# Kernel optimization log

Measured on AMD Instinct MI355X. Metric: run time of the kernel, lower is better.

## Reference

```python
import jax, jax.numpy as jnp
import numpy as np

B, N, DIM = 2, 2048, 1024
HEADS, DIM_HEAD = 16, 64
INNER = HEADS * DIM_HEAD  # 1024


def setup_inputs() -> dict:
    key = jax.random.key(0)
    k1, k2, k3, k4 = jax.random.split(key, 4)
    x = jax.random.normal(k1, (B, N, DIM), dtype=jnp.float32)
    # Linear weights (stored as [in, out] so y = x @ W)
    Wq = jax.random.normal(k2, (DIM, INNER), dtype=jnp.float32) * (DIM ** -0.5)
    Wkv = jax.random.normal(k3, (DIM, INNER * 2), dtype=jnp.float32) * (DIM ** -0.5)
    Wo = jax.random.normal(k4, (INNER, DIM), dtype=jnp.float32) * (INNER ** -0.5)
    return {"x": x, "Wq": Wq, "Wkv": Wkv, "Wo": Wo}


def reference(x, Wq, Wkv, Wo):
    # q/k/v projections (no bias), split heads: b n (h d) -> b h n d
    b, n, _ = x.shape
    q = (x @ Wq).reshape(b, n, HEADS, DIM_HEAD).transpose(0, 2, 1, 3)
    kv = x @ Wkv
    k, v = jnp.split(kv, 2, axis=-1)
    k = k.reshape(b, n, HEADS, DIM_HEAD).transpose(0, 2, 1, 3)
    v = v.reshape(b, n, HEADS, DIM_HEAD).transpose(0, 2, 1, 3)

    scale = DIM_HEAD ** -0.5
    scores = jnp.einsum('bhid,bhjd->bhij', q, k) * scale  # [b,h,n,n]
    # causal mask: positions j > i masked with most-negative value (as in torch impl)
    max_neg = -jnp.finfo(scores.dtype).max
    causal_mask = jnp.triu(jnp.ones((n, n), dtype=bool), k=1)
    scores = jnp.where(causal_mask, max_neg, scores)
    p = jax.nn.softmax(scores, axis=-1)
    out = jnp.einsum('bhij,bhjd->bhid', p, v)  # [b,h,n,d]
    out = out.transpose(0, 2, 1, 3).reshape(b, n, INNER)
    return out @ Wo
```

## Files before the change

kernel.cpp:

```cpp
#include <hip/hip_runtime.h>
#include <cstdint>


typedef __bf16 bf16_t;
typedef __bf16 bf16x8 __attribute__((ext_vector_type(8)));
typedef __bf16 bf16x4 __attribute__((ext_vector_type(4)));
typedef float  f32x4  __attribute__((ext_vector_type(4)));
typedef float  f32x16 __attribute__((ext_vector_type(16)));
typedef unsigned int u32;

#define QSCALE 0.18033688011112042f


__device__ __forceinline__ float fast_exp2(float x) {
#if __has_builtin(__builtin_amdgcn_exp2f)
  return __builtin_amdgcn_exp2f(x);
#else
  return exp2f(x);
#endif
}

__device__ __forceinline__ void swap32(u32& a, u32& b) {
#if __has_builtin(__builtin_amdgcn_permlane32_swap)
  typedef unsigned int u32x2 __attribute__((ext_vector_type(2)));
  const u32x2 r = __builtin_amdgcn_permlane32_swap(a, b, false, false);
  a = r[0]; b = r[1];
#else
  const u32 xa = (u32)__shfl_xor((int)a, 32, 64);
  const u32 xb = (u32)__shfl_xor((int)b, 32, 64);
  const bool hi = (threadIdx.x & 32) != 0;
  const u32 r0 = hi ? xb : a;
  const u32 r1 = hi ? b : xa;
  a = r0; b = r1;
#endif
}

__device__ __forceinline__ void gload_lds16(const void* gsrc, void* ldst) {
  __builtin_amdgcn_global_load_lds(
      (__attribute__((address_space(1))) void*)(uintptr_t)gsrc,
      (__attribute__((address_space(3))) void*)(uintptr_t)(uint32_t)(uintptr_t)ldst,
      16, 0, 0);
}

__device__ __forceinline__ u32 pkbf(float a, float b) {
  const u32 lo = (u32)__builtin_bit_cast(unsigned short, (bf16_t)a);
  const u32 hi = (u32)__builtin_bit_cast(unsigned short, (bf16_t)b);
  return (hi << 16) | lo;
}

__global__ __launch_bounds__(256) void cvt_kernel(const float* __restrict__ in,
                                                  bf16_t* __restrict__ out) {
  const int idx = (blockIdx.x * 256 + threadIdx.x) * 4;
  const float4 v = *(const float4*)(in + idx);
  bf16x4 o;
  o[0] = (bf16_t)v.x; o[1] = (bf16_t)v.y; o[2] = (bf16_t)v.z; o[3] = (bf16_t)v.w;
  *(bf16x4*)(out + idx) = o;
}

__global__ __launch_bounds__(256) void transpose_kernel(const float* __restrict__ W,
                                                        bf16_t* __restrict__ Wt,
                                                        int K, int Nn) {
  __shared__ float tile[32][33];
  const int bx = blockIdx.x, by = blockIdx.y;
  const int x = bx * 32 + threadIdx.x;
  #pragma unroll
  for (int r0 = 0; r0 < 32; r0 += 8) {
    const int r = r0 + threadIdx.y;
    tile[r][threadIdx.x] = W[(size_t)(by * 32 + r) * Nn + x];
  }
  __syncthreads();
  const int xo = by * 32 + threadIdx.x;
  #pragma unroll
  for (int r0 = 0; r0 < 32; r0 += 8) {
    const int r = r0 + threadIdx.y;
    Wt[(size_t)(bx * 32 + r) * K + xo] = (bf16_t)tile[threadIdx.x][r];
  }
}

template <int MODE>
__global__ __launch_bounds__(256) void gemm_kernel(
    const bf16_t* __restrict__ A, const bf16_t* __restrict__ Bt,
    bf16_t* __restrict__ outQ, bf16_t* __restrict__ outK,
    bf16_t* __restrict__ outV, float* __restrict__ outf) {
  constexpr int KD = 1024;
  __shared__ bf16_t As[2][128][64];
  __shared__ bf16_t Bs[2][128][64];
  const int t = threadIdx.x;
  const int lane = t & 63, w = t >> 6;
  const int wr = w >> 1, wc = w & 1;
  const int lrow = lane & 15, lq = lane >> 4;
  const int bm = blockIdx.y * 128, bn = blockIdx.x * 128;

  f32x4 acc[4][4] = {};

  auto stage = [&](int buf, int k0) {
    #pragma unroll
    for (int i = 0; i < 4; ++i) {
      const int lin = i * 256 + t;
      const int row = lin >> 3;
      const int sc = (lin & 7) ^ (row & 7);
      gload_lds16(A + (size_t)(bm + row) * KD + k0 + sc * 8,
                  &As[buf][0][0] + lin * 8);
      gload_lds16(Bt + (size_t)(bn + row) * KD + k0 + sc * 8,
                  &Bs[buf][0][0] + lin * 8);
    }
  };

  stage(0, 0);
  for (int kt = 0; kt < KD / 64; ++kt) {
    const int cur = kt & 1;
    if (kt + 1 < KD / 64) {
      stage(cur ^ 1, (kt + 1) * 64);
      asm volatile("s_waitcnt vmcnt(8)" ::: "memory");
    } else {
      asm volatile("s_waitcnt vmcnt(0)" ::: "memory");
    }
    __builtin_amdgcn_s_barrier();

    #pragma unroll
    for (int kk = 0; kk < 2; ++kk) {
      bf16x8 aF[4], bF[4];
      #pragma unroll
      for (int m = 0; m < 4; ++m) {
        const int row = wr * 64 + m * 16 + lrow;
        const int ch = (kk * 4 + lq) ^ (row & 7);
        aF[m] = *(const bf16x8*)&As[cur][row][ch * 8];
      }
      #pragma unroll
      for (int n = 0; n < 4; ++n) {
        const int row = wc * 64 + n * 16 + lrow;
        const int ch = (kk * 4 + lq) ^ (row & 7);
        bF[n] = *(const bf16x8*)&Bs[cur][row][ch * 8];
      }
      #pragma unroll
      for (int m = 0; m < 4; ++m)
        #pragma unroll
        for (int n = 0; n < 4; ++n)
          acc[m][n] = __builtin_amdgcn_mfma_f32_16x16x32_bf16(aF[m], bF[n],
                                                              acc[m][n], 0, 0, 0);
    }
    asm volatile("s_waitcnt lgkmcnt(0)" ::: "memory");
    __builtin_amdgcn_s_barrier();
  }

  #pragma unroll
  for (int m = 0; m < 4; ++m) {
    const int ri = bm + wr * 64 + m * 16 + lq * 4;
    #pragma unroll
    for (int n = 0; n < 4; ++n) {
      const int ci = bn + wc * 64 + n * 16 + lrow;
      const f32x4 v = acc[m][n];
      if (MODE == 2) {
        #pragma unroll
        for (int r = 0; r < 4; ++r)
          outf[(size_t)(ri + r) * 1024 + ci] = v[r];
      } else {
        if (ci < 2048) {
          const int cc = ci & 1023;
          const int h = cc >> 6, d = cc & 63;
          bf16_t* dst = (ci < 1024) ? outQ : outK;
          const float sc = (ci < 1024) ? QSCALE : 1.0f;
          const int fpart = (d >> 4) * 2;
          const int lpart = ((d >> 3) & 1) * 32;
          const int epart = d & 7;
          #pragma unroll
          for (int r = 0; r < 4; ++r) {
            const int i = ri + r;
            const int b = i >> 11, q = i & 2047;
            const size_t elem = (size_t)(b * 16 + h) * 131072
                + (size_t)((q >> 6) * 8 + fpart + ((q >> 5) & 1)) * 512
                + (lpart + (q & 31)) * 8 + epart;
            dst[elem] = (bf16_t)(v[r] * sc);
          }
        } else {
          const int hd = ci - 2048;
          const int h = hd >> 6, d = hd & 63;
          const int b = ri >> 11, j0 = ri & 2047;
          bf16x4 pk;
          pk[0] = (bf16_t)v[0]; pk[1] = (bf16_t)v[1];
          pk[2] = (bf16_t)v[2]; pk[3] = (bf16_t)v[3];
          const size_t elem = (size_t)(b * 16 + h) * 131072
              + (size_t)((j0 >> 6) * 8 + ((j0 & 63) >> 4) * 2 + (d >> 5)) * 512
              + ((((j0 >> 3) & 1) * 32) + (d & 31)) * 8 + (j0 & 7);
          *(bf16x4*)(outV + elem) = pk;
        }
      }
    }
  }
}

__global__ void __attribute__((amdgpu_flat_work_group_size(128, 128),
                               amdgpu_waves_per_eu(4, 4)))
attn_kernel(
    const bf16_t* __restrict__ Qf, const bf16_t* __restrict__ Kf,
    const bf16_t* __restrict__ Vf, bf16_t* __restrict__ Ow) {
  const int t = threadIdx.x;
  const int lane = t & 63, w = t >> 6;
  const int l31 = lane & 31, hi = lane >> 5;
  const int G = ((blockIdx.x & 7) << 8) + (blockIdx.x >> 3);
  const int bh = G >> 6;
  const int qs = 63 - (G & 63);
  const int qg = qs * 32 + l31;
  const bf16_t* Qb = Qf + (size_t)bh * 131072 + (size_t)(qs >> 1) * 4096 + (qs & 1) * 512;
  const bf16_t* Kb = Kf + (size_t)bh * 131072;
  const bf16_t* Vb = Vf + (size_t)bh * 131072;

  bf16x8 qf[4];
  #pragma unroll
  for (int ks = 0; ks < 4; ++ks)
    qf[ks] = *(const bf16x8*)(Qb + ks * 1024 + lane * 8);

  f32x16 acc0 = {}, acc1 = {};
  float m_run = -1e30f, l_half = 0.f;
  const int nt = (qs >> 1) + 1;

  for (int jt = w; jt < nt; jt += 2) {
    const bf16_t* Kt = Kb + (size_t)jt * 4096;
    const bf16_t* Vt = Vb + (size_t)jt * 4096;

    bf16x8 kc[8];
    #pragma unroll
    for (int f = 0; f < 8; ++f)
      kc[f] = *(const bf16x8*)(Kt + f * 512 + lane * 8);

    f32x16 st0 = {}, st1 = {};
    #pragma unroll
    for (int ks = 0; ks < 4; ++ks) {
      st0 = __builtin_amdgcn_mfma_f32_32x32x16_bf16(kc[2 * ks], qf[ks], st0, 0, 0, 0);
      st1 = __builtin_amdgcn_mfma_f32_32x32x16_bf16(kc[2 * ks + 1], qf[ks], st1, 0, 0, 0);
    }

    if (jt == nt - 1) {
      const int thr = qg - jt * 64;
      #pragma unroll
      for (int r = 0; r < 16; ++r) {
        const int jl = (r & 3) + 8 * (r >> 2) + 4 * hi;
        st0[r] = (jl > thr) ? -1e30f : st0[r];
        st1[r] = (32 + jl > thr) ? -1e30f : st1[r];
      }
    }

    float t8[8];
    #pragma unroll
    for (int i = 0; i < 8; ++i)
      t8[i] = fmaxf(fmaxf(st0[i], st0[i + 8]), fmaxf(st1[i], st1[i + 8]));
    #pragma unroll
    for (int i = 0; i < 4; ++i) t8[i] = fmaxf(t8[i], t8[i + 4]);
    const float pmax = fmaxf(fmaxf(t8[0], t8[1]), fmaxf(t8[2], t8[3]));

    if (!__all(pmax <= m_run + 8.0f)) {
      const float mx = fmaxf(pmax, __shfl_xor(pmax, 32, 64));
      const float m_new = fmaxf(m_run, mx);
      const float corr = fast_exp2(m_run - m_new);
      m_run = m_new;
      l_half *= corr;
      #pragma unroll
      for (int r = 0; r < 16; ++r) { acc0[r] *= corr; acc1[r] *= corr; }
    }

    #pragma unroll
    for (int r = 0; r < 16; ++r) {
      st0[r] = fast_exp2(st0[r] - m_run);
      st1[r] = fast_exp2(st1[r] - m_run);
    }
    float s8[8];
    #pragma unroll
    for (int i = 0; i < 8; ++i)
      s8[i] = (st0[i] + st0[i + 8]) + (st1[i] + st1[i + 8]);
    #pragma unroll
    for (int i = 0; i < 4; ++i) s8[i] += s8[i + 4];
    l_half += (s8[0] + s8[1]) + (s8[2] + s8[3]);

    bf16x8 vf[8];
    #pragma unroll
    for (int f = 0; f < 8; ++f)
      vf[f] = *(const bf16x8*)(Vt + f * 512 + lane * 8);

    u32 Wa[8], Wb[8];
    #pragma unroll
    for (int g = 0; g < 8; ++g) {
      Wa[g] = pkbf(st0[2 * g], st0[2 * g + 1]);
      Wb[g] = pkbf(st1[2 * g], st1[2 * g + 1]);
    }
    swap32(Wa[0], Wa[2]); swap32(Wa[1], Wa[3]);
    swap32(Wa[4], Wa[6]); swap32(Wa[5], Wa[7]);
    swap32(Wb[0], Wb[2]); swap32(Wb[1], Wb[3]);
    swap32(Wb[4], Wb[6]); swap32(Wb[5], Wb[7]);
    const uint4 u0 = make_uint4(Wa[0], Wa[1], Wa[2], Wa[3]);
    const uint4 u1 = make_uint4(Wa[4], Wa[5], Wa[6], Wa[7]);
    const uint4 u2 = make_uint4(Wb[0], Wb[1], Wb[2], Wb[3]);
    const uint4 u3 = make_uint4(Wb[4], Wb[5], Wb[6], Wb[7]);
    const bf16x8 pf0 = __builtin_bit_cast(bf16x8, u0);
    const bf16x8 pf1 = __builtin_bit_cast(bf16x8, u1);
    const bf16x8 pf2 = __builtin_bit_cast(bf16x8, u2);
    const bf16x8 pf3 = __builtin_bit_cast(bf16x8, u3);

    #pragma unroll
    for (int tt = 0; tt < 4; ++tt) {
      const bf16x8 pf = tt == 0 ? pf0 : tt == 1 ? pf1 : tt == 2 ? pf2 : pf3;
      acc0 = __builtin_amdgcn_mfma_f32_32x32x16_bf16(vf[2 * tt], pf, acc0, 0, 0, 0);
      acc1 = __builtin_amdgcn_mfma_f32_32x32x16_bf16(vf[2 * tt + 1], pf, acc1, 0, 0, 0);
    }
  }

  const float l_wave = l_half + __shfl_xor(l_half, 32, 64);

  __shared__ float mO[32][64];
  __shared__ float mML[2][64];
  if (w == 1) {
    mML[0][lane] = m_run;
    mML[1][lane] = l_wave;
    #pragma unroll
    for (int r = 0; r < 16; ++r) {
      mO[r][lane] = acc0[r];
      mO[16 + r][lane] = acc1[r];
    }
  }
  __syncthreads();
  if (w == 0) {
    const float m1 = mML[0][lane], l1 = mML[1][lane];
    const float mt = fmaxf(m_run, m1);
    const float c0 = fast_exp2(m_run - mt), c1 = fast_exp2(m1 - mt);
    const float l = l_wave * c0 + l1 * c1;
    const float inv = 1.0f / l;
    const int b = bh >> 4, h = bh & 15;
    bf16_t* Obase = Ow + (((size_t)(b * 2048 + qg)) << 10) + h * 64;
    #pragma unroll
    for (int g = 0; g < 4; ++g) {
      bf16x4 p0, p1;
      #pragma unroll
      for (int j = 0; j < 4; ++j) {
        p0[j] = (bf16_t)((acc0[4 * g + j] * c0 + mO[4 * g + j][lane] * c1) * inv);
        p1[j] = (bf16_t)((acc1[4 * g + j] * c0 + mO[16 + 4 * g + j][lane] * c1) * inv);
      }
      *(bf16x4*)(Obase + 8 * g + 4 * hi) = p0;
      *(bf16x4*)(Obase + 32 + 8 * g + 4 * hi) = p1;
    }
  }
}

extern "C" void kernel_launch(void* const* d_in, const int* in_sizes, int n_in,
                              void* d_out, int out_size, void* d_ws, size_t ws_size,
                              hipStream_t stream) {
  const float* x   = (const float*)d_in[0];
  const float* Wq  = (const float*)d_in[1];
  const float* Wkv = (const float*)d_in[2];
  const float* Wo  = (const float*)d_in[3];
  float* out = (float*)d_out;
  char* ws = (char*)d_ws;

  const size_t MB = 1024 * 1024;
  bf16_t* Xbf   = (bf16_t*)(ws);
  bf16_t* Wqkvt = (bf16_t*)(ws + 8 * MB);
  bf16_t* Wot   = (bf16_t*)(ws + 14 * MB);
  bf16_t* Qw    = (bf16_t*)(ws + 16 * MB);
  bf16_t* Kw    = (bf16_t*)(ws + 24 * MB);
  bf16_t* Vtw   = (bf16_t*)(ws + 32 * MB);
  bf16_t* Aw    = (bf16_t*)(ws + 40 * MB);

  cvt_kernel<<<4096, 256, 0, stream>>>(x, Xbf);
  dim3 tb(32, 8);
  transpose_kernel<<<dim3(32, 32), tb, 0, stream>>>(Wq, Wqkvt, 1024, 1024);
  transpose_kernel<<<dim3(64, 32), tb, 0, stream>>>(Wkv, Wqkvt + 1024 * 1024, 1024, 2048);
  transpose_kernel<<<dim3(32, 32), tb, 0, stream>>>(Wo, Wot, 1024, 1024);

  gemm_kernel<1><<<dim3(24, 32), 256, 0, stream>>>(Xbf, Wqkvt, Qw, Kw, Vtw, nullptr);
  attn_kernel<<<2048, 128, 0, stream>>>(Qw, Kw, Vtw, Aw);
  gemm_kernel<2><<<dim3(8, 32), 256, 0, stream>>>(Aw, Wot, nullptr, nullptr, nullptr, out);
}
```

Baseline: 114.9 us.

## Pair long and short causal query tiles per block with proportional wave split

Each 256-thread block now handles two complementary query tiles (qs = 63-p and p) of the same head. Its four waves are split between the two tiles in proportion to their key-tile counts, and each tile's partial softmax state is merged in shared memory by a leader wave. This balances causal work across blocks and gives each tile more waves, which should cut tail imbalance. The cost is a larger shared-memory footprint and a more complex reduction, and the rounding of the wave split can still leave some imbalance.

```diff
diff --git a/kernel.cpp b/kernel.cpp
--- a/kernel.cpp
+++ b/kernel.cpp
@@ -189,7 +189,7 @@
   }
 }
 
-__global__ void __attribute__((amdgpu_flat_work_group_size(128, 128),
+__global__ void __attribute__((amdgpu_flat_work_group_size(256, 256),
                                amdgpu_waves_per_eu(4, 4)))
 attn_kernel(
     const bf16_t* __restrict__ Qf, const bf16_t* __restrict__ Kf,
@@ -197,9 +197,17 @@
   const int t = threadIdx.x;
   const int lane = t & 63, w = t >> 6;
   const int l31 = lane & 31, hi = lane >> 5;
-  const int G = ((blockIdx.x & 7) << 8) + (blockIdx.x >> 3);
-  const int bh = G >> 6;
-  const int qs = 63 - (G & 63);
+  const int G = ((blockIdx.x & 7) << 7) + (blockIdx.x >> 3);
+  const int bh = G >> 5;
+  const int p = G & 31;
+  const int qsA = 63 - p, qsB = p;
+  const int ntA = (qsA >> 1) + 1, ntB = (qsB >> 1) + 1;
+  const int wA = min(3, (4 * ntA + ((ntA + ntB) >> 1)) / (ntA + ntB));
+  const bool isA = (w < wA);
+  const int qs = isA ? qsA : qsB;
+  const int nt = isA ? ntA : ntB;
+  const int widx = isA ? w : (w - wA);
+  const int ws = isA ? wA : (4 - wA);
   const int qg = qs * 32 + l31;
   const bf16_t* Qb = Qf + (size_t)bh * 131072 + (size_t)(qs >> 1) * 4096 + (qs & 1) * 512;
   const bf16_t* Kb = Kf + (size_t)bh * 131072;
@@ -212,9 +220,8 @@
 
   f32x16 acc0 = {}, acc1 = {};
   float m_run = -1e30f, l_half = 0.f;
-  const int nt = (qs >> 1) + 1;
-
-  for (int jt = w; jt < nt; jt += 2) {
+
+  for (int jt = widx; jt < nt; jt += ws) {
     const bf16_t* Kt = Kb + (size_t)jt * 4096;
     const bf16_t* Vt = Vb + (size_t)jt * 4096;
 
@@ -305,23 +312,36 @@
 
   const float l_wave = l_half + __shfl_xor(l_half, 32, 64);
 
-  __shared__ float mO[32][64];
-  __shared__ float mML[2][64];
-  if (w == 1) {
-    mML[0][lane] = m_run;
-    mML[1][lane] = l_wave;
+  __shared__ float mO[2][32][64];
+  __shared__ float mML[2][2][64];
+  const bool leader = (w == 0) || (w == wA);
+  if (!leader) {
+    const int slot = isA ? (w - 1) : (wA - 1 + (w - wA - 1));
+    mML[0][slot][lane] = m_run;
+    mML[1][slot][lane] = l_wave;
     #pragma unroll
     for (int r = 0; r < 16; ++r) {
-      mO[r][lane] = acc0[r];
-      mO[16 + r][lane] = acc1[r];
+      mO[slot][r][lane] = acc0[r];
+      mO[slot][16 + r][lane] = acc1[r];
     }
   }
   __syncthreads();
-  if (w == 0) {
-    const float m1 = mML[0][lane], l1 = mML[1][lane];
-    const float mt = fmaxf(m_run, m1);
-    const float c0 = fast_exp2(m_run - mt), c1 = fast_exp2(m1 - mt);
-    const float l = l_wave * c0 + l1 * c1;
+  if (leader) {
+    const int base = isA ? 0 : (wA - 1);
+    const int nsl = ws - 1;
+    float mk[2], lk[2], ck[2];
+    float mt = m_run;
+    for (int k = 0; k < nsl; ++k) {
+      mk[k] = mML[0][base + k][lane];
+      lk[k] = mML[1][base + k][lane];
+      mt = fmaxf(mt, mk[k]);
+    }
+    const float c0 = fast_exp2(m_run - mt);
+    float l = l_wave * c0;
+    for (int k = 0; k < nsl; ++k) {
+      ck[k] = fast_exp2(mk[k] - mt);
+      l += lk[k] * ck[k];
+    }
     const float inv = 1.0f / l;
     const int b = bh >> 4, h = bh & 15;
     bf16_t* Obase = Ow + (((size_t)(b * 2048 + qg)) << 10) + h * 64;
@@ -330,8 +350,14 @@
       bf16x4 p0, p1;
       #pragma unroll
       for (int j = 0; j < 4; ++j) {
-        p0[j] = (bf16_t)((acc0[4 * g + j] * c0 + mO[4 * g + j][lane] * c1) * inv);
-        p1[j] = (bf16_t)((acc1[4 * g + j] * c0 + mO[16 + 4 * g + j][lane] * c1) * inv);
+        float a0 = acc0[4 * g + j] * c0;
+        float a1 = acc1[4 * g + j] * c0;
+        for (int k = 0; k < nsl; ++k) {
+          a0 += mO[base + k][4 * g + j][lane] * ck[k];
+          a1 += mO[base + k][16 + 4 * g + j][lane] * ck[k];
+        }
+        p0[j] = (bf16_t)(a0 * inv);
+        p1[j] = (bf16_t)(a1 * inv);
       }
       *(bf16x4*)(Obase + 8 * g + 4 * hi) = p0;
       *(bf16x4*)(Obase + 32 + 8 * g + 4 * hi) = p1;
@@ -365,6 +391,6 @@
   transpose_kernel<<<dim3(32, 32), tb, 0, stream>>>(Wo, Wot, 1024, 1024);
 
   gemm_kernel<1><<<dim3(24, 32), 256, 0, stream>>>(Xbf, Wqkvt, Qw, Kw, Vtw, nullptr);
-  attn_kernel<<<2048, 128, 0, stream>>>(Qw, Kw, Vtw, Aw);
+  attn_kernel<<<1024, 256, 0, stream>>>(Qw, Kw, Vtw, Aw);
   gemm_kernel<2><<<dim3(8, 32), 256, 0, stream>>>(Aw, Wot, nullptr, nullptr, nullptr, out);
 }
```

Measured after the change: 107.4 us. 1.07x faster.
